# Kernel optimization log

Hardware: AMD Instinct MI355X
Metric: run time of the kernel (lower is better)

## Reference

```python
import jax, jax.numpy as jnp
import numpy as np

D_MODEL = 1024
NUM_HEADS = 16
D_K = D_MODEL // NUM_HEADS
THETA = 10000.0
BATCH = 2
SEQ = 2048


def _trunc_normal(key, shape, std):
    # approximate trunc_normal init; exact init distribution is irrelevant for correctness
    return jnp.clip(jax.random.normal(key, shape) * std, -3.0 * std, 3.0 * std)


def setup_inputs() -> dict:
    key = jax.random.key(0)
    ks = jax.random.split(key, 6)
    std = np.sqrt(2.0 / (D_MODEL + D_MODEL)).astype(np.float32)
    x = jax.random.normal(ks[0], (BATCH, SEQ, D_MODEL), dtype=jnp.float32)
    token_positions = jnp.tile(jnp.arange(SEQ, dtype=jnp.int32), (BATCH, 1))
    wq = _trunc_normal(ks[1], (D_MODEL, D_MODEL), std)  # (out, in)
    wk = _trunc_normal(ks[2], (D_MODEL, D_MODEL), std)
    wv = _trunc_normal(ks[3], (D_MODEL, D_MODEL), std)
    wo = _trunc_normal(ks[4], (D_MODEL, D_MODEL), std)
    return {"in_features": x, "wq": wq, "wk": wk, "wv": wv, "wo": wo,
            "token_positions": token_positions}


def _apply_rope(x, token_positions):
    # x: (B, H, S, d_k); token_positions: (B, S)
    half = D_K // 2
    inv_freq = 1.0 / (THETA ** (2.0 * jnp.arange(half, dtype=jnp.float32) / D_K))
    ang = token_positions.astype(jnp.float32)[..., None] * inv_freq  # (B, S, half)
    cos = jnp.cos(ang)[:, None, :, :]  # (B, 1, S, half) broadcast over heads
    sin = jnp.sin(ang)[:, None, :, :]
    x_even = x[..., 0::2]
    x_odd = x[..., 1::2]
    rot_even = x_even * cos - x_odd * sin
    rot_odd = x_even * sin + x_odd * cos
    return jnp.stack([rot_even, rot_odd], axis=-1).reshape(x.shape)


def reference(in_features, wq, wk, wv, wo, token_positions):
    B, S, _ = in_features.shape
    # bias-free linear: weight is (out, in)
    q = jnp.einsum('bsi,oi->bso', in_features, wq)
    k = jnp.einsum('bsi,oi->bso', in_features, wk)
    v = jnp.einsum('bsi,oi->bso', in_features, wv)
    # split heads: (B, H, S, d_k)
    def split(t):
        return t.reshape(B, S, NUM_HEADS, D_K).transpose(0, 2, 1, 3)
    qh, kh, vh = split(q), split(k), split(v)
    qh = _apply_rope(qh, token_positions)
    kh = _apply_rope(kh, token_positions)
    scale = 1.0 / jnp.sqrt(jnp.float32(D_K))
    logits = jnp.einsum('bhqd,bhkd->bhqk', qh, kh) * scale  # (B, H, S, S)
    causal = jnp.tril(jnp.ones((S, S), dtype=bool))
    logits = jnp.where(causal, logits, -jnp.inf)
    weights = jax.nn.softmax(logits, axis=-1)
    out = jnp.einsum('bhqk,bhkd->bhqd', weights, vh)  # (B, H, S, d_k)
    out = out.transpose(0, 2, 1, 3).reshape(B, S, D_MODEL)
    return jnp.einsum('bsi,oi->bso', out, wo)
```

## Files before the change

### kernel.cpp

```cpp
#include <hip/hip_runtime.h>
#include <hip/hip_bf16.h>
#include <math.h>

#define D_MODEL 1024
#define NUM_HEADS 16
#define DK 64
#define BATCH 2
#define SEQ 2048
#define NROWS (BATCH * SEQ)

typedef __bf16 bf16x8 __attribute__((ext_vector_type(8)));
typedef __bf16 bf16x4 __attribute__((ext_vector_type(4)));
typedef float f32x4 __attribute__((ext_vector_type(4)));

#define GLOAD_LDS16(g, l)                                          \
  __builtin_amdgcn_global_load_lds(                                \
      (const __attribute__((address_space(1))) void*)(g),          \
      (__attribute__((address_space(3))) void*)(l), 16, 0, 0)

#define LDS_FENCE() asm volatile("s_waitcnt lgkmcnt(0)" ::: "memory")

__global__ void cvt_all_kernel(const float* __restrict__ x,
                               const float* __restrict__ wq,
                               const float* __restrict__ wk,
                               const float* __restrict__ wv,
                               const float* __restrict__ wo,
                               __hip_bfloat16* __restrict__ xb,
                               __hip_bfloat16* __restrict__ wqkvb,
                               __hip_bfloat16* __restrict__ wob) {
  int t = blockIdx.x * 256 + threadIdx.x;
  const float* src;
  __hip_bfloat16* dst;
  int off;
  if (t < 1048576) {
    src = x; dst = xb; off = t;
  } else {
    int u = t - 1048576;
    int w = u >> 18;
    off = u & 262143;
    src = (w == 0) ? wq : (w == 1) ? wk : (w == 2) ? wv : wo;
    dst = (w < 3) ? (wqkvb + (size_t)w * 1048576) : wob;
  }
  float4 v = reinterpret_cast<const float4*>(src)[off];
  union { __hip_bfloat16 h[4]; uint2 u; } tmp;
  tmp.h[0] = __float2bfloat16(v.x);
  tmp.h[1] = __float2bfloat16(v.y);
  tmp.h[2] = __float2bfloat16(v.z);
  tmp.h[3] = __float2bfloat16(v.w);
  reinterpret_cast<uint2*>(dst)[off] = tmp.u;
}

__global__ __launch_bounds__(256)
void gemm_qkv_kernel(const __hip_bfloat16* __restrict__ A,
                     const __hip_bfloat16* __restrict__ W,
                     __hip_bfloat16* __restrict__ O0,
                     __hip_bfloat16* __restrict__ O1,
                     __hip_bfloat16* __restrict__ O2) {
  __shared__ __hip_bfloat16 sA[2][128 * 32];
  __shared__ __hip_bfloat16 sB[2][128 * 32];
  const int tid = threadIdx.x;
  const int wave = tid >> 6, lane = tid & 63, quad = lane >> 4, l16 = lane & 15;
  const int wm = (wave >> 1) * 64, wn = (wave & 1) * 64;
  const int bm = blockIdx.x * 128;
  const int bnG = blockIdx.y * 128;
  int which = blockIdx.y >> 3;
  __hip_bfloat16* O = (which == 0) ? O0 : (which == 1) ? O1 : O2;
  const int ocol = bnG & 1023;
  const int srow = lane >> 2, scol = (lane & 3) * 8;

#pragma unroll
  for (int c = 0; c < 2; ++c) {
    int ch = wave + c * 4;
    GLOAD_LDS16(&A[(size_t)(bm + ch * 16 + srow) * D_MODEL + scol], &sA[0][ch * 512]);
    GLOAD_LDS16(&W[(size_t)(bnG + ch * 16 + srow) * D_MODEL + scol], &sB[0][ch * 512]);
  }

  f32x4 acc[4][4] = {};
  for (int it = 0; it < 32; ++it) {
    __syncthreads();
    if (it + 1 < 32) {
      const int k0 = (it + 1) * 32, nb = (it + 1) & 1;
#pragma unroll
      for (int c = 0; c < 2; ++c) {
        int ch = wave + c * 4;
        GLOAD_LDS16(&A[(size_t)(bm + ch * 16 + srow) * D_MODEL + k0 + scol],
                    &sA[nb][ch * 512]);
        GLOAD_LDS16(&W[(size_t)(bnG + ch * 16 + srow) * D_MODEL + k0 + scol],
                    &sB[nb][ch * 512]);
      }
    }
    const int cb = it & 1;
    bf16x8 af[4], bfb[4];
#pragma unroll
    for (int i = 0; i < 4; ++i)
      af[i] = *reinterpret_cast<bf16x8*>(&sA[cb][(wm + i * 16 + l16) * 32 + quad * 8]);
#pragma unroll
    for (int j = 0; j < 4; ++j)
      bfb[j] = *reinterpret_cast<bf16x8*>(&sB[cb][(wn + j * 16 + l16) * 32 + quad * 8]);
#pragma unroll
    for (int i = 0; i < 4; ++i)
#pragma unroll
      for (int j = 0; j < 4; ++j)
        acc[i][j] = __builtin_amdgcn_mfma_f32_16x16x32_bf16(af[i], bfb[j], acc[i][j], 0, 0, 0);
  }

#pragma unroll
  for (int i = 0; i < 4; ++i)
#pragma unroll
    for (int j = 0; j < 4; ++j)
#pragma unroll
      for (int r = 0; r < 4; ++r) {
        int row = bm + wm + i * 16 + quad * 4 + r;
        int col = ocol + wn + j * 16 + l16;
        O[(size_t)row * D_MODEL + col] = __float2bfloat16(acc[i][j][r]);
      }
}

__global__ __launch_bounds__(256)
void gemm_out_kernel(const __hip_bfloat16* __restrict__ A,
                     const __hip_bfloat16* __restrict__ W,
                     float* __restrict__ O) {
  __shared__ __hip_bfloat16 sA[2][64 * 32];
  __shared__ __hip_bfloat16 sB[2][128 * 32];
  const int tid = threadIdx.x;
  const int wave = tid >> 6, lane = tid & 63, quad = lane >> 4, l16 = lane & 15;
  const int mh = (wave >> 1) * 32, nh = (wave & 1) * 64;
  const int bm = blockIdx.x * 64, bn = blockIdx.y * 128;
  const int srow = lane >> 2, scol = (lane & 3) * 8;

  GLOAD_LDS16(&A[(size_t)(bm + wave * 16 + srow) * D_MODEL + scol], &sA[0][wave * 512]);
#pragma unroll
  for (int c = 0; c < 2; ++c) {
    int ch = wave + c * 4;
    GLOAD_LDS16(&W[(size_t)(bn + ch * 16 + srow) * D_MODEL + scol], &sB[0][ch * 512]);
  }

  f32x4 acc[2][4] = {};
  for (int it = 0; it < 32; ++it) {
    __syncthreads();
    if (it + 1 < 32) {
      const int k0 = (it + 1) * 32, nb = (it + 1) & 1;
      GLOAD_LDS16(&A[(size_t)(bm + wave * 16 + srow) * D_MODEL + k0 + scol],
                  &sA[nb][wave * 512]);
#pragma unroll
      for (int c = 0; c < 2; ++c) {
        int ch = wave + c * 4;
        GLOAD_LDS16(&W[(size_t)(bn + ch * 16 + srow) * D_MODEL + k0 + scol],
                    &sB[nb][ch * 512]);
      }
    }
    const int cb = it & 1;
    bf16x8 af[2], bfb[4];
#pragma unroll
    for (int i = 0; i < 2; ++i)
      af[i] = *reinterpret_cast<bf16x8*>(&sA[cb][(mh + i * 16 + l16) * 32 + quad * 8]);
#pragma unroll
    for (int j = 0; j < 4; ++j)
      bfb[j] = *reinterpret_cast<bf16x8*>(&sB[cb][(nh + j * 16 + l16) * 32 + quad * 8]);
#pragma unroll
    for (int i = 0; i < 2; ++i)
#pragma unroll
      for (int j = 0; j < 4; ++j)
        acc[i][j] = __builtin_amdgcn_mfma_f32_16x16x32_bf16(af[i], bfb[j], acc[i][j], 0, 0, 0);
  }

#pragma unroll
  for (int i = 0; i < 2; ++i)
#pragma unroll
    for (int j = 0; j < 4; ++j)
#pragma unroll
      for (int r = 0; r < 4; ++r) {
        int row = bm + mh + i * 16 + quad * 4 + r;
        int col = bn + nh + j * 16 + l16;
        O[(size_t)row * D_MODEL + col] = acc[i][j][r];
      }
}

__global__ void rope_kernel(__hip_bfloat16* __restrict__ Q,
                            __hip_bfloat16* __restrict__ K,
                            const int* __restrict__ pos) {
  constexpr float QS = 0.18033688011112042f;
  int t = blockIdx.x * 256 + threadIdx.x;
  int row = t >> 7;
  int c = t & 127;
  int h = c >> 3, co = (c & 7) * 8;
  float ps = (float)pos[row];
  size_t off = (size_t)row * D_MODEL + h * DK + co;
  bf16x8 q = *reinterpret_cast<const bf16x8*>(&Q[off]);
  bf16x8 k = *reinterpret_cast<const bf16x8*>(&K[off]);
#pragma unroll
  for (int j = 0; j < 4; ++j) {
    float p = (float)((co >> 1) + j);
    float ang = ps * exp2f(-p * 0.41524101186091903f);
    float cs = cosf(ang), sn = sinf(ang);
    float qe = (float)q[2 * j], qo = (float)q[2 * j + 1];
    q[2 * j]     = (__bf16)((qe * cs - qo * sn) * QS);
    q[2 * j + 1] = (__bf16)((qe * sn + qo * cs) * QS);
    float ke = (float)k[2 * j], ko = (float)k[2 * j + 1];
    k[2 * j]     = (__bf16)(ke * cs - ko * sn);
    k[2 * j + 1] = (__bf16)(ke * sn + ko * cs);
  }
  *reinterpret_cast<bf16x8*>(&Q[off]) = q;
  *reinterpret_cast<bf16x8*>(&K[off]) = k;
}

__global__ __launch_bounds__(256)
void attn_kernel(const __hip_bfloat16* __restrict__ Q,
                 const __hip_bfloat16* __restrict__ K,
                 const __hip_bfloat16* __restrict__ V,
                 __hip_bfloat16* __restrict__ Ao) {
  constexpr int LS = 66;
  __shared__ __hip_bfloat16 sK[2][64 * LS];
  __shared__ __hip_bfloat16 sVt[2][64 * LS];
  __shared__ __hip_bfloat16 sPt[4][16 * 64];
  const int tid = threadIdx.x;
  const int wave = tid >> 6, lane = tid & 63, quad = lane >> 4, l16 = lane & 15;
  const int idx = blockIdx.x;
  const int bh = idx & 31;
  const int half = (idx >> 5) & 1;
  const int pi = idx >> 6;
  const int qlo = pi, qhi = 15 - pi;
  const int h = bh & 15, b = bh >> 4;
  const int ho = h * DK;
  const size_t rowbase = (size_t)b * SEQ;
  const int jL = half * 4 + wave, jU = 7 - jL;
  const int sbs[2] = {qlo * 128 + jL * 16, qhi * 128 + jU * 16};
  const int nt = ((qhi * 128 + (7 - half * 4) * 16 + 15) >> 6) + 1;
  const __hip_bfloat16* Kbase = K + rowbase * D_MODEL + ho;
  const unsigned short* Vu =
      reinterpret_cast<const unsigned short*>(V + rowbase * D_MODEL + ho);

  bf16x8 aq[2][2];
#pragma unroll
  for (int s = 0; s < 2; ++s)
#pragma unroll
    for (int kk = 0; kk < 2; ++kk)
      aq[s][kk] = *reinterpret_cast<const bf16x8*>(
          &Q[(rowbase + sbs[s] + l16) * D_MODEL + ho + kk * 32 + quad * 8]);

  f32x4 o_acc[2][4] = {};
  float l_run[2] = {0.f, 0.f};

  const int krow = tid >> 2, kc = (tid & 3) * 16;

  {
    *reinterpret_cast<bf16x8*>(&sK[0][krow * LS + kc]) =
        *reinterpret_cast<const bf16x8*>(&Kbase[(size_t)krow * D_MODEL + kc]);
    *reinterpret_cast<bf16x8*>(&sK[0][krow * LS + kc + 8]) =
        *reinterpret_cast<const bf16x8*>(&Kbase[(size_t)krow * D_MODEL + kc + 8]);
#pragma unroll
    for (int c = 0; c < 8; ++c) {
      int u = c * 256 + tid;
      int d = u & 63, kvp = u >> 6;
      unsigned lo = Vu[(size_t)(2 * kvp) * D_MODEL + d];
      unsigned hi = Vu[(size_t)(2 * kvp + 1) * D_MODEL + d];
      *reinterpret_cast<unsigned*>(&sVt[0][d * LS + 2 * kvp]) = lo | (hi << 16);
    }
  }

  for (int t = 0; t < nt; ++t) {
    __syncthreads();
    const int buf = t & 1;
    const bool hn = (t + 1) < nt;
    bf16x8 kn0, kn1;
    unsigned vw[8];
    if (hn) {
      const int kvn = (t + 1) * 64;
      kn0 = *reinterpret_cast<const bf16x8*>(
          &Kbase[(size_t)(kvn + krow) * D_MODEL + kc]);
      kn1 = *reinterpret_cast<const bf16x8*>(
          &Kbase[(size_t)(kvn + krow) * D_MODEL + kc + 8]);
#pragma unroll
      for (int c = 0; c < 8; ++c) {
        int u = c * 256 + tid;
        int d = u & 63, kvp = u >> 6;
        unsigned lo = Vu[(size_t)(kvn + 2 * kvp) * D_MODEL + d];
        unsigned hi = Vu[(size_t)(kvn + 2 * kvp + 1) * D_MODEL + d];
        vw[c] = lo | (hi << 16);
      }
    }

    const int kv0 = t * 64;
    if (kv0 <= sbs[1] + 15) {
      bf16x8 ak[2][4], bv[2][4];
#pragma unroll
      for (int kk = 0; kk < 2; ++kk)
#pragma unroll
        for (int j = 0; j < 4; ++j) {
          ak[kk][j] = *reinterpret_cast<bf16x8*>(
              &sK[buf][(j * 16 + l16) * LS + kk * 32 + quad * 8]);
          bv[kk][j] = *reinterpret_cast<bf16x8*>(
              &sVt[buf][(j * 16 + l16) * LS + kk * 32 + quad * 8]);
        }

#pragma unroll
      for (int s = 0; s < 2; ++s) {
        const int sb = sbs[s];
        if (kv0 > sb + 15) continue;
        f32x4 sv[4] = {};
#pragma unroll
        for (int kk = 0; kk < 2; ++kk)
#pragma unroll
          for (int j = 0; j < 4; ++j)
            sv[j] = __builtin_amdgcn_mfma_f32_16x16x32_bf16(ak[kk][j], aq[s][kk],
                                                            sv[j], 0, 0, 0);
        if (kv0 + 63 > sb) {
#pragma unroll
          for (int j = 0; j < 4; ++j)
#pragma unroll
            for (int r = 0; r < 4; ++r)
              if (kv0 + j * 16 + quad * 4 + r > sb + l16) sv[j][r] = -INFINITY;
        }
        float ls = 0.f;
#pragma unroll
        for (int j = 0; j < 4; ++j) {
          bf16x4 pk;
#pragma unroll
          for (int r = 0; r < 4; ++r) {
            float p = __builtin_amdgcn_exp2f(sv[j][r]);
            ls += p;
            pk[r] = (__bf16)p;
          }
          int wgr = (2 * j + (quad >> 1)) ^ (l16 & 7);
          *reinterpret_cast<bf16x4*>(
              &sPt[wave][l16 * 64 + wgr * 8 + (quad & 1) * 4]) = pk;
        }
        l_run[s] += ls;
        LDS_FENCE();
#pragma unroll
        for (int kk = 0; kk < 2; ++kk) {
          int rgr = (4 * kk + quad) ^ (l16 & 7);
          bf16x8 ap = *reinterpret_cast<bf16x8*>(&sPt[wave][l16 * 64 + rgr * 8]);
#pragma unroll
          for (int jd = 0; jd < 4; ++jd)
            o_acc[s][jd] = __builtin_amdgcn_mfma_f32_16x16x32_bf16(
                ap, bv[kk][jd], o_acc[s][jd], 0, 0, 0);
        }
      }
    }

    if (hn) {
      const int nb = buf ^ 1;
      *reinterpret_cast<bf16x8*>(&sK[nb][krow * LS + kc]) = kn0;
      *reinterpret_cast<bf16x8*>(&sK[nb][krow * LS + kc + 8]) = kn1;
#pragma unroll
      for (int c = 0; c < 8; ++c) {
        int u = c * 256 + tid;
        int d = u & 63, kvp = u >> 6;
        *reinterpret_cast<unsigned*>(&sVt[nb][d * LS + 2 * kvp]) = vw[c];
      }
    }
  }

#pragma unroll
  for (int s = 0; s < 2; ++s) {
    float l = l_run[s];
    l += __shfl_xor(l, 16);
    l += __shfl_xor(l, 32);
    __hip_bfloat16* Aobase = Ao + (rowbase + sbs[s]) * D_MODEL + ho;
#pragma unroll
    for (int r = 0; r < 4; ++r) {
      float linv = 1.0f / __shfl(l, quad * 4 + r);
#pragma unroll
      for (int jd = 0; jd < 4; ++jd)
        Aobase[(size_t)(quad * 4 + r) * D_MODEL + jd * 16 + l16] =
            __float2bfloat16(o_acc[s][jd][r] * linv);
    }
  }
}

extern "C" void kernel_launch(void* const* d_in, const int* in_sizes, int n_in,
                              void* d_out, int out_size, void* d_ws, size_t ws_size,
                              hipStream_t stream) {
  const float* x = (const float*)d_in[0];
  const float* wq = (const float*)d_in[1];
  const float* wk = (const float*)d_in[2];
  const float* wv = (const float*)d_in[3];
  const float* wo = (const float*)d_in[4];
  const int* tpos = (const int*)d_in[5];
  float* out = (float*)d_out;
  char* ws = (char*)d_ws;

  __hip_bfloat16* xb    = (__hip_bfloat16*)(ws);
  __hip_bfloat16* wqkvb = (__hip_bfloat16*)(ws + (size_t)(8)  * 1048576);
  __hip_bfloat16* wob   = (__hip_bfloat16*)(ws + (size_t)(14) * 1048576);
  __hip_bfloat16* Qb    = (__hip_bfloat16*)(ws + (size_t)(16) * 1048576);
  __hip_bfloat16* Kb    = (__hip_bfloat16*)(ws + (size_t)(24) * 1048576);
  __hip_bfloat16* Vb    = (__hip_bfloat16*)(ws + (size_t)(32) * 1048576);
  __hip_bfloat16* Aob   = xb;

  cvt_all_kernel<<<8192, 256, 0, stream>>>(x, wq, wk, wv, wo, xb, wqkvb, wob);

  gemm_qkv_kernel<<<dim3(32, 24), 256, 0, stream>>>(xb, wqkvb, Qb, Kb, Vb);

  rope_kernel<<<2048, 256, 0, stream>>>(Qb, Kb, tpos);

  attn_kernel<<<512, 256, 0, stream>>>(Qb, Kb, Vb, Aob);

  gemm_out_kernel<<<dim3(64, 8), 256, 0, stream>>>(Aob, wob, out);
}
```

Measured before the change: 205.6 us.

## Write V transposed from QKV GEMM and XOR-swizzle attention LDS tiles

```diff
diff --git a/kernel.cpp b/kernel.cpp
--- a/kernel.cpp
+++ b/kernel.cpp
@@ -55,24 +55,24 @@
                      const __hip_bfloat16* __restrict__ W,
                      __hip_bfloat16* __restrict__ O0,
                      __hip_bfloat16* __restrict__ O1,
-                     __hip_bfloat16* __restrict__ O2) {
-  __shared__ __hip_bfloat16 sA[2][128 * 32];
-  __shared__ __hip_bfloat16 sB[2][128 * 32];
+                     __hip_bfloat16* __restrict__ Vt) {
+  __shared__ __hip_bfloat16 smem[2][2][128 * 32];
+#define sAg(b) (smem[0][b])
+#define sBg(b) (smem[1][b])
   const int tid = threadIdx.x;
   const int wave = tid >> 6, lane = tid & 63, quad = lane >> 4, l16 = lane & 15;
   const int wm = (wave >> 1) * 64, wn = (wave & 1) * 64;
   const int bm = blockIdx.x * 128;
   const int bnG = blockIdx.y * 128;
-  int which = blockIdx.y >> 3;
-  __hip_bfloat16* O = (which == 0) ? O0 : (which == 1) ? O1 : O2;
+  const int which = blockIdx.y >> 3;
   const int ocol = bnG & 1023;
   const int srow = lane >> 2, scol = (lane & 3) * 8;
 
 #pragma unroll
   for (int c = 0; c < 2; ++c) {
     int ch = wave + c * 4;
-    GLOAD_LDS16(&A[(size_t)(bm + ch * 16 + srow) * D_MODEL + scol], &sA[0][ch * 512]);
-    GLOAD_LDS16(&W[(size_t)(bnG + ch * 16 + srow) * D_MODEL + scol], &sB[0][ch * 512]);
+    GLOAD_LDS16(&A[(size_t)(bm + ch * 16 + srow) * D_MODEL + scol], &sAg(0)[ch * 512]);
+    GLOAD_LDS16(&W[(size_t)(bnG + ch * 16 + srow) * D_MODEL + scol], &sBg(0)[ch * 512]);
   }
 
   f32x4 acc[4][4] = {};
@@ -84,19 +84,19 @@
       for (int c = 0; c < 2; ++c) {
         int ch = wave + c * 4;
         GLOAD_LDS16(&A[(size_t)(bm + ch * 16 + srow) * D_MODEL + k0 + scol],
-                    &sA[nb][ch * 512]);
+                    &sAg(nb)[ch * 512]);
         GLOAD_LDS16(&W[(size_t)(bnG + ch * 16 + srow) * D_MODEL + k0 + scol],
-                    &sB[nb][ch * 512]);
+                    &sBg(nb)[ch * 512]);
       }
     }
     const int cb = it & 1;
     bf16x8 af[4], bfb[4];
 #pragma unroll
     for (int i = 0; i < 4; ++i)
-      af[i] = *reinterpret_cast<bf16x8*>(&sA[cb][(wm + i * 16 + l16) * 32 + quad * 8]);
+      af[i] = *reinterpret_cast<bf16x8*>(&sAg(cb)[(wm + i * 16 + l16) * 32 + quad * 8]);
 #pragma unroll
     for (int j = 0; j < 4; ++j)
-      bfb[j] = *reinterpret_cast<bf16x8*>(&sB[cb][(wn + j * 16 + l16) * 32 + quad * 8]);
+      bfb[j] = *reinterpret_cast<bf16x8*>(&sBg(cb)[(wn + j * 16 + l16) * 32 + quad * 8]);
 #pragma unroll
     for (int i = 0; i < 4; ++i)
 #pragma unroll
@@ -104,16 +104,49 @@
         acc[i][j] = __builtin_amdgcn_mfma_f32_16x16x32_bf16(af[i], bfb[j], acc[i][j], 0, 0, 0);
   }
 
-#pragma unroll
-  for (int i = 0; i < 4; ++i)
-#pragma unroll
-    for (int j = 0; j < 4; ++j)
-#pragma unroll
-      for (int r = 0; r < 4; ++r) {
-        int row = bm + wm + i * 16 + quad * 4 + r;
-        int col = ocol + wn + j * 16 + l16;
-        O[(size_t)row * D_MODEL + col] = __float2bfloat16(acc[i][j][r]);
+  if (which < 2) {
+    __hip_bfloat16* O = (which == 0) ? O0 : O1;
+#pragma unroll
+    for (int i = 0; i < 4; ++i)
+#pragma unroll
+      for (int j = 0; j < 4; ++j)
+#pragma unroll
+        for (int r = 0; r < 4; ++r) {
+          int row = bm + wm + i * 16 + quad * 4 + r;
+          int col = ocol + wn + j * 16 + l16;
+          O[(size_t)row * D_MODEL + col] = __float2bfloat16(acc[i][j][r]);
+        }
+  } else {
+    __syncthreads();
+    __hip_bfloat16* tr = &smem[0][0][0];
+#pragma unroll
+    for (int i = 0; i < 4; ++i)
+#pragma unroll
+      for (int j = 0; j < 4; ++j) {
+        int c = wn + j * 16 + l16;
+        int r = wm + i * 16 + quad * 4;
+        bf16x4 pk;
+#pragma unroll
+        for (int rr = 0; rr < 4; ++rr) pk[rr] = (__bf16)acc[i][j][rr];
+        int g = (r >> 3) ^ (c & 15);
+        *reinterpret_cast<bf16x4*>(&tr[c * 128 + g * 8 + (r & 7)]) = pk;
       }
+    __syncthreads();
+    int c = tid >> 1;
+    int vcol = ocol + c;
+    int hh = vcol >> 6, dd = vcol & 63;
+    int bb = bm >> 11, s0 = (bm & 2047) + (tid & 1) * 64;
+    __hip_bfloat16* dst = Vt + ((size_t)(bb * 16 + hh) * 64 + dd) * 2048 + s0;
+    int gbase = (tid & 1) * 8;
+#pragma unroll
+    for (int k = 0; k < 8; ++k) {
+      int g = (gbase + k) ^ (c & 15);
+      *reinterpret_cast<bf16x8*>(&dst[k * 8]) =
+          *reinterpret_cast<bf16x8*>(&tr[c * 128 + g * 8]);
+    }
+  }
+#undef sAg
+#undef sBg
 }
 
 __global__ __launch_bounds__(256)
@@ -207,11 +240,10 @@
 __global__ __launch_bounds__(256)
 void attn_kernel(const __hip_bfloat16* __restrict__ Q,
                  const __hip_bfloat16* __restrict__ K,
-                 const __hip_bfloat16* __restrict__ V,
+                 const __hip_bfloat16* __restrict__ Vt,
                  __hip_bfloat16* __restrict__ Ao) {
-  constexpr int LS = 66;
-  __shared__ __hip_bfloat16 sK[2][64 * LS];
-  __shared__ __hip_bfloat16 sVt[2][64 * LS];
+  __shared__ __hip_bfloat16 sK[2][64 * 64];
+  __shared__ __hip_bfloat16 sVt[2][64 * 64];
   __shared__ __hip_bfloat16 sPt[4][16 * 64];
   const int tid = threadIdx.x;
   const int wave = tid >> 6, lane = tid & 63, quad = lane >> 4, l16 = lane & 15;
@@ -227,8 +259,7 @@
   const int sbs[2] = {qlo * 128 + jL * 16, qhi * 128 + jU * 16};
   const int nt = ((qhi * 128 + (7 - half * 4) * 16 + 15) >> 6) + 1;
   const __hip_bfloat16* Kbase = K + rowbase * D_MODEL + ho;
-  const unsigned short* Vu =
-      reinterpret_cast<const unsigned short*>(V + rowbase * D_MODEL + ho);
+  const __hip_bfloat16* Vtbase = Vt + (size_t)(b * 16 + h) * 64 * 2048;
 
   bf16x8 aq[2][2];
 #pragma unroll
@@ -241,43 +272,36 @@
   f32x4 o_acc[2][4] = {};
   float l_run[2] = {0.f, 0.f};
 
-  const int krow = tid >> 2, kc = (tid & 3) * 16;
+  const int srow = tid >> 2, sc = (tid & 3) * 16;
+  const int ga = (tid & 3) * 2;
+  const int sga = (ga ^ (srow & 7)) * 8, sgb = ((ga + 1) ^ (srow & 7)) * 8;
 
   {
-    *reinterpret_cast<bf16x8*>(&sK[0][krow * LS + kc]) =
-        *reinterpret_cast<const bf16x8*>(&Kbase[(size_t)krow * D_MODEL + kc]);
-    *reinterpret_cast<bf16x8*>(&sK[0][krow * LS + kc + 8]) =
-        *reinterpret_cast<const bf16x8*>(&Kbase[(size_t)krow * D_MODEL + kc + 8]);
-#pragma unroll
-    for (int c = 0; c < 8; ++c) {
-      int u = c * 256 + tid;
-      int d = u & 63, kvp = u >> 6;
-      unsigned lo = Vu[(size_t)(2 * kvp) * D_MODEL + d];
-      unsigned hi = Vu[(size_t)(2 * kvp + 1) * D_MODEL + d];
-      *reinterpret_cast<unsigned*>(&sVt[0][d * LS + 2 * kvp]) = lo | (hi << 16);
-    }
+    bf16x8 k0 = *reinterpret_cast<const bf16x8*>(&Kbase[(size_t)srow * D_MODEL + sc]);
+    bf16x8 k1 = *reinterpret_cast<const bf16x8*>(&Kbase[(size_t)srow * D_MODEL + sc + 8]);
+    bf16x8 v0 = *reinterpret_cast<const bf16x8*>(&Vtbase[(size_t)srow * 2048 + sc]);
+    bf16x8 v1 = *reinterpret_cast<const bf16x8*>(&Vtbase[(size_t)srow * 2048 + sc + 8]);
+    *reinterpret_cast<bf16x8*>(&sK[0][srow * 64 + sga]) = k0;
+    *reinterpret_cast<bf16x8*>(&sK[0][srow * 64 + sgb]) = k1;
+    *reinterpret_cast<bf16x8*>(&sVt[0][srow * 64 + sga]) = v0;
+    *reinterpret_cast<bf16x8*>(&sVt[0][srow * 64 + sgb]) = v1;
   }
 
   for (int t = 0; t < nt; ++t) {
     __syncthreads();
     const int buf = t & 1;
     const bool hn = (t + 1) < nt;
-    bf16x8 kn0, kn1;
-    unsigned vw[8];
+    bf16x8 kn0, kn1, vn0, vn1;
     if (hn) {
       const int kvn = (t + 1) * 64;
       kn0 = *reinterpret_cast<const bf16x8*>(
-          &Kbase[(size_t)(kvn + krow) * D_MODEL + kc]);
+          &Kbase[(size_t)(kvn + srow) * D_MODEL + sc]);
       kn1 = *reinterpret_cast<const bf16x8*>(
-          &Kbase[(size_t)(kvn + krow) * D_MODEL + kc + 8]);
-#pragma unroll
-      for (int c = 0; c < 8; ++c) {
-        int u = c * 256 + tid;
-        int d = u & 63, kvp = u >> 6;
-        unsigned lo = Vu[(size_t)(kvn + 2 * kvp) * D_MODEL + d];
-        unsigned hi = Vu[(size_t)(kvn + 2 * kvp + 1) * D_MODEL + d];
-        vw[c] = lo | (hi << 16);
-      }
+          &Kbase[(size_t)(kvn + srow) * D_MODEL + sc + 8]);
+      vn0 = *reinterpret_cast<const bf16x8*>(
+          &Vtbase[(size_t)srow * 2048 + kvn + sc]);
+      vn1 = *reinterpret_cast<const bf16x8*>(
+          &Vtbase[(size_t)srow * 2048 + kvn + sc + 8]);
     }
 
     const int kv0 = t * 64;
@@ -287,10 +311,9 @@
       for (int kk = 0; kk < 2; ++kk)
 #pragma unroll
         for (int j = 0; j < 4; ++j) {
-          ak[kk][j] = *reinterpret_cast<bf16x8*>(
-              &sK[buf][(j * 16 + l16) * LS + kk * 32 + quad * 8]);
-          bv[kk][j] = *reinterpret_cast<bf16x8*>(
-              &sVt[buf][(j * 16 + l16) * LS + kk * 32 + quad * 8]);
+          int go = ((4 * kk + quad) ^ (l16 & 7)) * 8;
+          ak[kk][j] = *reinterpret_cast<bf16x8*>(&sK[buf][(j * 16 + l16) * 64 + go]);
+          bv[kk][j] = *reinterpret_cast<bf16x8*>(&sVt[buf][(j * 16 + l16) * 64 + go]);
         }
 
 #pragma unroll
@@ -341,14 +364,10 @@
 
     if (hn) {
       const int nb = buf ^ 1;
-      *reinterpret_cast<bf16x8*>(&sK[nb][krow * LS + kc]) = kn0;
-      *reinterpret_cast<bf16x8*>(&sK[nb][krow * LS + kc + 8]) = kn1;
-#pragma unroll
-      for (int c = 0; c < 8; ++c) {
-        int u = c * 256 + tid;
-        int d = u & 63, kvp = u >> 6;
-        *reinterpret_cast<unsigned*>(&sVt[nb][d * LS + 2 * kvp]) = vw[c];
-      }
+      *reinterpret_cast<bf16x8*>(&sK[nb][srow * 64 + sga]) = kn0;
+      *reinterpret_cast<bf16x8*>(&sK[nb][srow * 64 + sgb]) = kn1;
+      *reinterpret_cast<bf16x8*>(&sVt[nb][srow * 64 + sga]) = vn0;
+      *reinterpret_cast<bf16x8*>(&sVt[nb][srow * 64 + sgb]) = vn1;
     }
   }
 
@@ -386,16 +405,16 @@
   __hip_bfloat16* wob   = (__hip_bfloat16*)(ws + (size_t)(14) * 1048576);
   __hip_bfloat16* Qb    = (__hip_bfloat16*)(ws + (size_t)(16) * 1048576);
   __hip_bfloat16* Kb    = (__hip_bfloat16*)(ws + (size_t)(24) * 1048576);
-  __hip_bfloat16* Vb    = (__hip_bfloat16*)(ws + (size_t)(32) * 1048576);
+  __hip_bfloat16* Vtb   = (__hip_bfloat16*)(ws + (size_t)(32) * 1048576);
   __hip_bfloat16* Aob   = xb;
 
   cvt_all_kernel<<<8192, 256, 0, stream>>>(x, wq, wk, wv, wo, xb, wqkvb, wob);
 
-  gemm_qkv_kernel<<<dim3(32, 24), 256, 0, stream>>>(xb, wqkvb, Qb, Kb, Vb);
+  gemm_qkv_kernel<<<dim3(32, 24), 256, 0, stream>>>(xb, wqkvb, Qb, Kb, Vtb);
 
   rope_kernel<<<2048, 256, 0, stream>>>(Qb, Kb, tpos);
 
-  attn_kernel<<<512, 256, 0, stream>>>(Qb, Kb, Vb, Aob);
+  attn_kernel<<<512, 256, 0, stream>>>(Qb, Kb, Vtb, Aob);
 
   gemm_out_kernel<<<dim3(64, 8), 256, 0, stream>>>(Aob, wob, out);
 }
```

Result: faster. 182.4 us (-11.3%).
